# Kernel tuning notes

Measured on AMD Instinct MI355X. Metric: run time of the kernel, lower is better.

Reference implementation:

```python
import jax, jax.numpy as jnp
import numpy as np

N_NODES = 100000
N_EDGES = 800000
# (in_dim, out_channels_per_head, heads) for the 5 stacked GATConv layers
DIMS = [(32, 24, 10), (240, 24, 5), (120, 24, 2), (48, 24, 1), (24, 12, 1)]
NEG_SLOPE = 0.2  # PyG GATConv default leaky_relu slope


def setup_inputs() -> dict:
    key = jax.random.key(0)
    ks = jax.random.split(key, 4 + 4 * len(DIMS))
    x = jax.random.normal(ks[0], (N_NODES, 32), jnp.float32)
    # edge_index with no self loops (dst = src + nonzero offset mod N),
    # since PyG GATConv removes then re-adds self loops.
    src = jax.random.randint(ks[1], (N_EDGES,), 0, N_NODES)
    off = jax.random.randint(ks[2], (N_EDGES,), 1, N_NODES)
    dst = (src + off) % N_NODES
    edge_index = jnp.stack([src, dst]).astype(jnp.int32)
    edge_attr = jax.random.normal(ks[3], (N_EDGES, 4), jnp.float32)
    inp = {"x": x, "edge_index": edge_index, "edge_attr": edge_attr}
    for i, (din, c, h) in enumerate(DIMS):
        kw, kb, ka, kd = ks[4 + 4 * i: 8 + 4 * i]
        s = 1.0 / np.sqrt(din)
        inp[f"W{i}"] = jax.random.normal(kw, (din, h * c), jnp.float32) * s
        inp[f"b{i}"] = jax.random.normal(kb, (h * c,), jnp.float32) * 0.01
        inp[f"as{i}"] = jax.random.normal(ka, (h, c), jnp.float32) * (1.0 / np.sqrt(c))
        inp[f"ad{i}"] = jax.random.normal(kd, (h, c), jnp.float32) * (1.0 / np.sqrt(c))
    return inp


def gat_layer(x, src, dst, W, b, a_src, a_dst):
    # Faithful PyG GATConv (concat=True, bias=True, edge_dim=None)
    n = x.shape[0]
    h_heads, c = a_src.shape
    h = (x @ W).reshape(n, h_heads, c)                      # [N,H,C]
    alpha_s = jnp.einsum('nhc,hc->nh', h, a_src)            # [N,H]
    alpha_d = jnp.einsum('nhc,hc->nh', h, a_dst)            # [N,H]
    e = jax.nn.leaky_relu(alpha_s[src] + alpha_d[dst], NEG_SLOPE)  # [E,H]
    # segment softmax over incoming edges of each destination node
    m = jax.ops.segment_max(e, dst, num_segments=n)         # [N,H]
    ex = jnp.exp(e - m[dst])
    z = jax.ops.segment_sum(ex, dst, num_segments=n)        # [N,H]
    attn = ex / z[dst]                                      # [E,H]
    out = jax.ops.segment_sum(h[src] * attn[:, :, None], dst, num_segments=n)
    return out.reshape(n, h_heads * c) + b


def reference(x, edge_index, edge_attr,
              W0, b0, as0, ad0, W1, b1, as1, ad1, W2, b2, as2, ad2,
              W3, b3, as3, ad3, W4, b4, as4, ad4):
    # edge_attr is ignored: GATConv(edge_dim=None) does not use it.
    n = x.shape[0]
    loop = jnp.arange(n, dtype=edge_index.dtype)
    src = jnp.concatenate([edge_index[0], loop])  # add self loops (PyG default)
    dst = jnp.concatenate([edge_index[1], loop])
    params = [(W0, b0, as0, ad0), (W1, b1, as1, ad1), (W2, b2, as2, ad2),
              (W3, b3, as3, ad3), (W4, b4, as4, ad4)]
    for W, b, a_s, a_d in params:
        x = jax.nn.relu(gat_layer(x, src, dst, W, b, a_s, a_d))
    return x
```

## Files before the change

kernel.cpp:

```cpp
#include <hip/hip_runtime.h>
#include <math.h>

#define NN 100000
#define EE 800000
#define ET (EE + NN)
#define BS 256
#define BKTS 391
#define FB_EPB 4096
#define LDSCAP 4096

typedef _Float16 f16;
typedef __attribute__((ext_vector_type(2))) _Float16 h2v;
typedef __attribute__((ext_vector_type(4))) _Float16 half4;
typedef __attribute__((ext_vector_type(8))) _Float16 half8;
typedef __attribute__((ext_vector_type(4))) float f32x4;
template<int V> struct HV;
template<> struct HV<4>{ typedef half4 type; };
template<> struct HV<8>{ typedef half8 type; };

static inline int cdiv(long a, int b){ return (int)((a + b - 1) / b); }

__global__ __launch_bounds__(256) void k_bhist(const int* __restrict__ ei,
                                               int* __restrict__ bucketCount){
    __shared__ int hist[BKTS];
    for (int t = threadIdx.x; t < BKTS; t += 256) hist[t] = 0;
    __syncthreads();
    const int e0 = blockIdx.x * FB_EPB + threadIdx.x;
    #pragma unroll
    for (int i = 0; i < 16; i++){
        int e = e0 + i * 256;
        if (e < ET){
            int d = (e < EE) ? ei[EE + e] : (e - EE);
            atomicAdd(&hist[d >> 8], 1);
        }
    }
    __syncthreads();
    for (int t = threadIdx.x; t < BKTS; t += 256){
        int c = hist[t];
        if (c) atomicAdd(&bucketCount[t], c);
    }
}

__global__ void k_bscan(const int* __restrict__ bucketCount, int* __restrict__ bucketBase,
                        int* __restrict__ bucketCursor, int* __restrict__ rowptr){
    __shared__ int sh[512];
    int t = threadIdx.x;
    int c = (t < BKTS) ? bucketCount[t] : 0;
    sh[t] = c;
    __syncthreads();
    for (int o = 1; o < 512; o <<= 1){
        int v = (t >= o) ? sh[t - o] : 0;
        __syncthreads();
        sh[t] += v;
        __syncthreads();
    }
    if (t < BKTS){
        int excl = sh[t] - c;
        bucketBase[t] = excl;
        bucketCursor[t] = excl;
    }
    if (t == 0){
        bucketBase[BKTS] = ET;
        rowptr[NN] = ET;
    }
}

__global__ __launch_bounds__(256) void k_bfill(const int* __restrict__ ei,
        int* __restrict__ bucketCursor, unsigned* __restrict__ bpack){
    __shared__ int hist[BKTS];
    __shared__ int base[BKTS];
    for (int t = threadIdx.x; t < BKTS; t += 256) hist[t] = 0;
    __syncthreads();
    const int e0 = blockIdx.x * FB_EPB + threadIdx.x;
    unsigned pk[16], rb[16];
    #pragma unroll
    for (int i = 0; i < 16; i++){
        int e = e0 + i * 256;
        rb[i] = 0xFFFFFFFFu;
        if (e < ET){
            int s, d;
            if (e < EE){ s = ei[e]; d = ei[EE + e]; } else { s = e - EE; d = s; }
            int b = d >> 8;
            int r = atomicAdd(&hist[b], 1);
            pk[i] = ((unsigned)(d & 255) << 17) | (unsigned)s;
            rb[i] = ((unsigned)r << 9) | (unsigned)b;
        }
    }
    __syncthreads();
    for (int t = threadIdx.x; t < BKTS; t += 256){
        int c = hist[t];
        base[t] = c ? atomicAdd(&bucketCursor[t], c) : 0;
    }
    __syncthreads();
    #pragma unroll
    for (int i = 0; i < 16; i++){
        if (rb[i] != 0xFFFFFFFFu){
            int b = rb[i] & 511;
            int r = rb[i] >> 9;
            bpack[base[b] + r] = pk[i];
        }
    }
}

__global__ __launch_bounds__(256) void k_bsort(const unsigned* __restrict__ bpack,
        const int* __restrict__ bucketBase, int* __restrict__ rowptr,
        int* __restrict__ ssrc){
    __shared__ int cnt[256];
    __shared__ int off[256];
    __shared__ unsigned stage[LDSCAP];
    int b = blockIdx.x;
    int n0 = bucketBase[b], n1 = bucketBase[b + 1];
    int nE = n1 - n0;
    int t = threadIdx.x;
    cnt[t] = 0;
    __syncthreads();
    for (int i = t; i < nE; i += 256){
        unsigned v = bpack[n0 + i];
        atomicAdd(&cnt[v >> 17], 1);
    }
    __syncthreads();
    int cv = cnt[t];
    off[t] = cv;
    __syncthreads();
    for (int o = 1; o < 256; o <<= 1){
        int v = (t >= o) ? off[t - o] : 0;
        __syncthreads();
        off[t] += v;
        __syncthreads();
    }
    int excl = off[t] - cv;
    __syncthreads();
    off[t] = excl;
    cnt[t] = 0;
    __syncthreads();
    for (int i = t; i < nE; i += 256){
        unsigned v = bpack[n0 + i];
        int dl = v >> 17;
        int r = atomicAdd(&cnt[dl], 1);
        stage[off[dl] + r] = v;
    }
    int d = b * 256 + t;
    if (d < NN) rowptr[d] = n0 + excl;
    __syncthreads();
    for (int i = t; i < nE; i += 256){
        unsigned v = stage[i];
        ssrc[n0 + i] = (int)(v & 0x1FFFFu);
    }
}

template<int K, int M, int KP, int MP, int HH, int CC>
__device__ __forceinline__ void prep_one(int idx, const float* __restrict__ W,
        const float* __restrict__ b, const float* __restrict__ as_,
        const float* __restrict__ ad_, f16* __restrict__ Wpk,
        float* __restrict__ bp, float* __restrict__ Was, float* __restrict__ Wad){
    constexpr int NT = MP / 16;
    if (idx < KP * MP){
        int j    = idx & 7;
        int lane = (idx >> 3) & 63;
        int rest = idx >> 9;
        int nt   = rest % NT;
        int ks   = rest / NT;
        int k = ks * 32 + ((lane >> 4) & 3) * 8 + j;
        int n = nt * 16 + (lane & 15);
        Wpk[idx] = (k < K && n < M) ? (f16)W[k * M + n] : (f16)0.f;
    }
    if (idx < MP) bp[idx] = (idx < M) ? b[idx] : 0.f;
    if (idx < K * HH){
        int k = idx / HH, hd = idx - k * HH;
        float s = 0.f, d = 0.f;
        #pragma unroll
        for (int c = 0; c < CC; c++){
            float w = W[k * M + hd * CC + c];
            s = fmaf(w, as_[hd * CC + c], s);
            d = fmaf(w, ad_[hd * CC + c], d);
        }
        Was[idx] = s;
        Wad[idx] = d;
    }
}

__device__ __forceinline__ void prep_w0(int idx, const float* __restrict__ W0,
                                        f16* __restrict__ Wpk0){
    int j    = idx & 7;
    int lane = (idx >> 3) & 63;
    int nt   = (idx >> 9) & 1;
    int hd   = idx >> 10;
    int k    = ((lane >> 4) & 3) * 8 + j;
    int cih  = nt * 16 + (lane & 15);
    Wpk0[idx] = (cih < 24) ? (f16)W0[k * 240 + hd * 24 + cih] : (f16)0.f;
}

struct PrepAll {
    const float *W[5], *b[5], *as[5], *ad[5];
    f16*   Wpk[5];
    f16*   Wpk0;
    float* bp[5];
    float* Was[5];
    float* Wad[5];
    int*   bucketCount;
};

__global__ void k_prep_all(PrepAll a){
    int idx = blockIdx.x * 256 + threadIdx.x;
    if (idx < 7680)
        prep_one< 32, 240,  32, 240, 10, 24>(idx,         a.W[0], a.b[0], a.as[0], a.ad[0], a.Wpk[0], a.bp[0], a.Was[0], a.Wad[0]);
    else if (idx < 40448)
        prep_one<240, 120, 256, 128,  5, 24>(idx - 7680,  a.W[1], a.b[1], a.as[1], a.ad[1], a.Wpk[1], a.bp[1], a.Was[1], a.Wad[1]);
    else if (idx < 48640)
        prep_one<120,  48, 128,  64,  2, 24>(idx - 40448, a.W[2], a.b[2], a.as[2], a.ad[2], a.Wpk[2], a.bp[2], a.Was[2], a.Wad[2]);
    else if (idx < 50688)
        prep_one< 48,  24,  64,  32,  1, 24>(idx - 48640, a.W[3], a.b[3], a.as[3], a.ad[3], a.Wpk[3], a.bp[3], a.Was[3], a.Wad[3]);
    else if (idx < 51200)
        prep_one< 24,  12,  32,  16,  1, 12>(idx - 50688, a.W[4], a.b[4], a.as[4], a.ad[4], a.Wpk[4], a.bp[4], a.Was[4], a.Wad[4]);
    else if (idx < 61440)
        prep_w0(idx - 51200, a.W[0], a.Wpk0);
    else if (idx < 61440 + BKTS)
        a.bucketCount[idx - 61440] = 0;
}

__global__ void k_cvt_alpha0(const float* __restrict__ X, f16* __restrict__ Xh,
                             const float* __restrict__ Was, const float* __restrict__ Wad,
                             float* __restrict__ als, float* __restrict__ ald){
    int n = blockIdx.x * BS + threadIdx.x;
    if (n >= NN) return;
    float xr[32];
    #pragma unroll
    for (int i = 0; i < 8; i++){
        float4 v = *(const float4*)(X + (long)n * 32 + i * 4);
        xr[i * 4 + 0] = v.x; xr[i * 4 + 1] = v.y;
        xr[i * 4 + 2] = v.z; xr[i * 4 + 3] = v.w;
    }
    #pragma unroll
    for (int i = 0; i < 4; i++){
        half8 h;
        #pragma unroll
        for (int c = 0; c < 8; c++) h[c] = (f16)xr[i * 8 + c];
        *(half8*)(Xh + (long)n * 32 + i * 8) = h;
    }
    float s[10] = {}, d[10] = {};
    for (int k = 0; k < 32; k++){
        float x = xr[k];
        #pragma unroll
        for (int hd = 0; hd < 10; hd++){
            s[hd] = fmaf(x, Was[k * 10 + hd], s[hd]);
            d[hd] = fmaf(x, Wad[k * 10 + hd], d[hd]);
        }
    }
    #pragma unroll
    for (int hd = 0; hd < 10; hd++){
        als[(long)n * 12 + hd] = s[hd];
        ald[(long)n * 12 + hd] = d[hd];
    }
}

template<int MPH, int HH, int CC, int SL>
__global__ void k_alpha_h(const f16* __restrict__ H2, const float* __restrict__ as_,
                          const float* __restrict__ ad_, float* __restrict__ als,
                          float* __restrict__ ald){
    int n = blockIdx.x * BS + threadIdx.x;
    if (n >= NN) return;
    const f16* h = H2 + (long)n * MPH;
    #pragma unroll
    for (int hd = 0; hd < HH; hd++){
        float s = 0.f, d = 0.f;
        #pragma unroll
        for (int c0 = 0; c0 < CC; c0 += 4){
            half4 hv = *(const half4*)(h + hd * CC + c0);
            #pragma unroll
            for (int j = 0; j < 4; j++){
                float hvf = (float)hv[j];
                s = fmaf(hvf, as_[hd * CC + c0 + j], s);
                d = fmaf(hvf, ad_[hd * CC + c0 + j], d);
            }
        }
        als[(long)n * SL + hd] = s;
        ald[(long)n * SL + hd] = d;
    }
}

__device__ __forceinline__ void smx_upd(float& ma, float& L, float& z, float e, float adv){
    float mn = fmaxf(ma, e);
    float Ln = mn + adv; Ln = (Ln >= 0.f) ? Ln : 0.2f * Ln;
    float ev = e + adv;  ev = (ev >= 0.f) ? ev : 0.2f * ev;
    z = z * __expf(L - Ln) + __expf(ev - Ln);
    ma = mn; L = Ln;
}

template<int HH, int SL, int ATTS, int TPN>
__global__ __launch_bounds__(256) void k_mzatt_split(const float* __restrict__ als,
        const float* __restrict__ ald, const int* __restrict__ rowptr,
        const int* __restrict__ ssrc, f16* __restrict__ att){
    constexpr int HPT = HH / TPN;
    long idx = (long)blockIdx.x * 256 + threadIdx.x;
    if (idx >= (long)NN * TPN) return;
    int n = (int)(idx / TPN);
    int g = (int)(idx - (long)n * TPN);
    const int c0 = g * HPT;
    float adv[HPT], ma[HPT], L[HPT], z[HPT];
    #pragma unroll
    for (int h = 0; h < HPT; h++){
        adv[h] = ald[(long)n * SL + c0 + h];
        ma[h] = -1e30f; L[h] = -1e30f; z[h] = 0.f;
    }
    const int beg = rowptr[n], end = rowptr[n + 1];
    int p = beg;
    for (; p + 4 <= end; p += 4){
        int s0 = ssrc[p], s1 = ssrc[p+1], s2 = ssrc[p+2], s3 = ssrc[p+3];
        float e0[HPT], e1[HPT], e2[HPT], e3[HPT];
        if constexpr (HPT == 2){
            float2 v0 = *(const float2*)(als + (long)s0 * SL + c0);
            float2 v1 = *(const float2*)(als + (long)s1 * SL + c0);
            float2 v2 = *(const float2*)(als + (long)s2 * SL + c0);
            float2 v3 = *(const float2*)(als + (long)s3 * SL + c0);
            e0[0]=v0.x; e0[1]=v0.y; e1[0]=v1.x; e1[1]=v1.y;
            e2[0]=v2.x; e2[1]=v2.y; e3[0]=v3.x; e3[1]=v3.y;
        } else {
            e0[0] = als[(long)s0 * SL + c0];
            e1[0] = als[(long)s1 * SL + c0];
            e2[0] = als[(long)s2 * SL + c0];
            e3[0] = als[(long)s3 * SL + c0];
        }
        #pragma unroll
        for (int h = 0; h < HPT; h++){
            smx_upd(ma[h], L[h], z[h], e0[h], adv[h]);
            smx_upd(ma[h], L[h], z[h], e1[h], adv[h]);
            smx_upd(ma[h], L[h], z[h], e2[h], adv[h]);
            smx_upd(ma[h], L[h], z[h], e3[h], adv[h]);
        }
    }
    for (; p < end; ++p){
        int s = ssrc[p];
        float e[HPT];
        if constexpr (HPT == 2){
            float2 v = *(const float2*)(als + (long)s * SL + c0);
            e[0] = v.x; e[1] = v.y;
        } else {
            e[0] = als[(long)s * SL + c0];
        }
        #pragma unroll
        for (int h = 0; h < HPT; h++) smx_upd(ma[h], L[h], z[h], e[h], adv[h]);
    }
    float zi[HPT];
    int pos[HPT];
    #pragma unroll
    for (int h = 0; h < HPT; h++){
        zi[h] = 1.f / z[h];
        int hh = c0 + h;
        pos[h] = (ATTS == 16) ? (hh + ((hh >= 5) ? 3 : 0)) : hh;
    }
    auto emit = [&](int pp, const float* e){
        #pragma unroll
        for (int h = 0; h < HPT; h++){
            float ev = e[h] + adv[h]; ev = (ev >= 0.f) ? ev : 0.2f * ev;
            att[(long)pp * ATTS + pos[h]] = (f16)(__expf(ev - L[h]) * zi[h]);
        }
    };
    p = beg;
    for (; p + 4 <= end; p += 4){
        int s0 = ssrc[p], s1 = ssrc[p+1], s2 = ssrc[p+2], s3 = ssrc[p+3];
        float e0[HPT], e1[HPT], e2[HPT], e3[HPT];
        if constexpr (HPT == 2){
            float2 v0 = *(const float2*)(als + (long)s0 * SL + c0);
            float2 v1 = *(const float2*)(als + (long)s1 * SL + c0);
            float2 v2 = *(const float2*)(als + (long)s2 * SL + c0);
            float2 v3 = *(const float2*)(als + (long)s3 * SL + c0);
            e0[0]=v0.x; e0[1]=v0.y; e1[0]=v1.x; e1[1]=v1.y;
            e2[0]=v2.x; e2[1]=v2.y; e3[0]=v3.x; e3[1]=v3.y;
        } else {
            e0[0] = als[(long)s0 * SL + c0];
            e1[0] = als[(long)s1 * SL + c0];
            e2[0] = als[(long)s2 * SL + c0];
            e3[0] = als[(long)s3 * SL + c0];
        }
        emit(p, e0); emit(p+1, e1); emit(p+2, e2); emit(p+3, e3);
    }
    for (; p < end; ++p){
        int s = ssrc[p];
        float e[HPT];
        if constexpr (HPT == 2){
            float2 v = *(const float2*)(als + (long)s * SL + c0);
            e[0] = v.x; e[1] = v.y;
        } else {
            e[0] = als[(long)s * SL + c0];
        }
        emit(p, e);
    }
}

__global__ __launch_bounds__(256) void k_aggX0_gemm(const f16* __restrict__ Xh,
        const f16* __restrict__ att, const int* __restrict__ rowptr,
        const int* __restrict__ ssrc, const f16* __restrict__ Wpk0,
        const float* __restrict__ bp0, f16* __restrict__ X1){
    constexpr int SA = 328;
    constexpr int SO = 264;
    __shared__ f16 smem[32 * SA];
    const int t = threadIdx.x;
    const long n0 = (long)blockIdx.x * 32;

    {
        const int nloc = t >> 3;
        const int hg   = (t >> 2) & 1;
        const int ch   = t & 3;
        const int n    = (int)n0 + nloc;
        float acc[5][8] = {};
        int beg = rowptr[n], end = rowptr[n + 1];
        int p = beg;
        for (; p + 4 <= end; p += 4){
            int s0 = ssrc[p], s1 = ssrc[p+1], s2 = ssrc[p+2], s3 = ssrc[p+3];
            half8 x0 = *(const half8*)(Xh + (long)s0 * 32 + ch * 8);
            half8 x1 = *(const half8*)(Xh + (long)s1 * 32 + ch * 8);
            half8 x2 = *(const half8*)(Xh + (long)s2 * 32 + ch * 8);
            half8 x3 = *(const half8*)(Xh + (long)s3 * 32 + ch * 8);
            half8 a0 = *(const half8*)(att + (long)p * 16 + hg * 8);
            half8 a1 = *(const half8*)(att + (long)(p+1) * 16 + hg * 8);
            half8 a2 = *(const half8*)(att + (long)(p+2) * 16 + hg * 8);
            half8 a3 = *(const half8*)(att + (long)(p+3) * 16 + hg * 8);
            #pragma unroll
            for (int h = 0; h < 5; h++){
                float w0 = (float)a0[h], w1 = (float)a1[h];
                float w2 = (float)a2[h], w3 = (float)a3[h];
                #pragma unroll
                for (int c = 0; c < 8; c++){
                    acc[h][c] = fmaf(w0, (float)x0[c], acc[h][c]);
                    acc[h][c] = fmaf(w1, (float)x1[c], acc[h][c]);
                    acc[h][c] = fmaf(w2, (float)x2[c], acc[h][c]);
                    acc[h][c] = fmaf(w3, (float)x3[c], acc[h][c]);
                }
            }
        }
        for (; p < end; ++p){
            int s = ssrc[p];
            half8 xv = *(const half8*)(Xh + (long)s * 32 + ch * 8);
            half8 av = *(const half8*)(att + (long)p * 16 + hg * 8);
            #pragma unroll
            for (int h = 0; h < 5; h++){
                float w = (float)av[h];
                #pragma unroll
                for (int c = 0; c < 8; c++)
                    acc[h][c] = fmaf(w, (float)xv[c], acc[h][c]);
            }
        }
        #pragma unroll
        for (int h = 0; h < 5; h++){
            half8 o;
            #pragma unroll
            for (int c = 0; c < 8; c++) o[c] = (f16)acc[h][c];
            *(half8*)(smem + nloc * SA + (hg * 5 + h) * 32 + ch * 8) = o;
        }
    }
    __syncthreads();

    const int wave = t >> 6;
    const int lane = t & 63;
    const int quad = lane >> 4;
    const int l16  = lane & 15;
    const int mt   = wave & 1;
    half8 afr[5];
    #pragma unroll
    for (int i = 0; i < 5; i++){
        const int hd = (wave + 4 * i) >> 1;
        afr[i] = *(const half8*)(smem + (mt * 16 + l16) * SA + hd * 32 + quad * 8);
    }
    __syncthreads();
    #pragma unroll
    for (int i = 0; i < 5; i++){
        const int hd = (wave + 4 * i) >> 1;
        #pragma unroll
        for (int nt = 0; nt < 2; nt++){
            half8 bfr = *(const half8*)(Wpk0 + ((hd * 2 + nt) * 64 + lane) * 8);
            f32x4 acc2 = (f32x4){0.f, 0.f, 0.f, 0.f};
            acc2 = __builtin_amdgcn_mfma_f32_16x16x32_f16(afr[i], bfr, acc2, 0, 0, 0);
            int cih = nt * 16 + l16;
            if (cih < 24){
                float bv = bp0[hd * 24 + cih];
                #pragma unroll
                for (int reg = 0; reg < 4; reg++){
                    int rl = mt * 16 + quad * 4 + reg;
                    float v = acc2[reg] + bv;
                    smem[rl * SO + hd * 24 + cih] = (f16)((v > 0.f) ? v : 0.f);
                }
            }
        }
    }
    __syncthreads();

    const half8 hz = {};
    #pragma unroll
    for (int c = t; c < 1024; c += 256){
        int row = c >> 5, c8 = c & 31;
        half8 v = (c8 >= 30) ? hz : *(const half8*)(smem + row * SO + c8 * 8);
        *(half8*)(X1 + (n0 + row) * 256 + c8 * 8) = v;
    }
}

template<int KP, int MPH>
__global__ __launch_bounds__(256) void k_gemm_mfma(const f16* __restrict__ Xh,
        const f16* __restrict__ Wpk, f16* __restrict__ H2){
    constexpr int NT = MPH / 16;
    constexpr int KS = KP / 32;
    const int wave = threadIdx.x >> 6;
    const int lane = threadIdx.x & 63;
    const int quad = lane >> 4;
    const int l16  = lane & 15;
    const long row0 = (long)blockIdx.x * 128 + wave * 32;

    f32x4 acc[2][NT];
    #pragma unroll
    for (int mt = 0; mt < 2; mt++)
        #pragma unroll
        for (int nt = 0; nt < NT; nt++)
            acc[mt][nt] = (f32x4){0.f, 0.f, 0.f, 0.f};

    const long r0 = row0 + l16;
    const long r1 = row0 + 16 + l16;
    const half8 hz = {};
    half8 a0 = (r0 < NN) ? *(const half8*)(Xh + r0 * KP + quad * 8) : hz;
    half8 a1 = (r1 < NN) ? *(const half8*)(Xh + r1 * KP + quad * 8) : hz;
    half8 bc[NT];
    #pragma unroll
    for (int nt = 0; nt < NT; nt++)
        bc[nt] = *(const half8*)(Wpk + ((long)nt * 64 + lane) * 8);

    for (int ks = 0; ks < KS; ks++){
        half8 n0 = hz, n1 = hz, bn[NT];
        if (ks + 1 < KS){
            const int kk = (ks + 1) * 32 + quad * 8;
            n0 = (r0 < NN) ? *(const half8*)(Xh + r0 * KP + kk) : hz;
            n1 = (r1 < NN) ? *(const half8*)(Xh + r1 * KP + kk) : hz;
            const f16* bp_ = Wpk + ((long)(ks + 1) * NT * 64 + lane) * 8;
            #pragma unroll
            for (int nt = 0; nt < NT; nt++)
                bn[nt] = *(const half8*)(bp_ + (long)nt * 512);
        } else {
            #pragma unroll
            for (int nt = 0; nt < NT; nt++) bn[nt] = hz;
        }
        #pragma unroll
        for (int nt = 0; nt < NT; nt++){
            acc[0][nt] = __builtin_amdgcn_mfma_f32_16x16x32_f16(a0, bc[nt], acc[0][nt], 0, 0, 0);
            acc[1][nt] = __builtin_amdgcn_mfma_f32_16x16x32_f16(a1, bc[nt], acc[1][nt], 0, 0, 0);
        }
        a0 = n0; a1 = n1;
        #pragma unroll
        for (int nt = 0; nt < NT; nt++) bc[nt] = bn[nt];
    }
    #pragma unroll
    for (int mt = 0; mt < 2; mt++){
        #pragma unroll
        for (int reg = 0; reg < 4; reg++){
            long r = row0 + mt * 16 + quad * 4 + reg;
            if (r < NN){
                #pragma unroll
                for (int nt = 0; nt < NT; nt++)
                    H2[r * MPH + nt * 16 + l16] = (f16)acc[mt][nt][reg];
            }
        }
    }
}

template<int HH, int CC, int ATTS, int MPH, int MPO, int VEC, bool O16>
__global__ __launch_bounds__(256) void k_agg_h(const f16* __restrict__ H2,
        const f16* __restrict__ att,
        const int* __restrict__ rowptr, const int* __restrict__ ssrc,
        const float* __restrict__ bp, f16* __restrict__ out16,
        float* __restrict__ out32, int MREAL){
    constexpr int TPN = MPO / VEC;
    typedef typename HV<VEC>::type hvec;
    int idx = blockIdx.x * 256 + threadIdx.x;
    if (idx >= NN * TPN) return;
    int n = idx / TPN;
    int q = idx - n * TPN;
    int j0 = q * VEC;
    if constexpr (O16 && (MPO > MPH)){
        if (j0 >= MPH){
            hvec zv = {};
            *(hvec*)(out16 + (long)n * MPO + j0) = zv;
            return;
        }
    }
    int hd = j0 / CC; if (hd > HH - 1) hd = HH - 1;

    int beg = rowptr[n], end = rowptr[n + 1];
    float acc[VEC] = {};
    int p = beg;
    for (; p + 2 <= end; p += 2){
        int s0 = ssrc[p], s1 = ssrc[p + 1];
        float w0 = (float)att[(long)p * ATTS + hd];
        float w1 = (float)att[(long)(p + 1) * ATTS + hd];
        hvec h0 = *(const hvec*)(H2 + (long)s0 * MPH + j0);
        hvec h1 = *(const hvec*)(H2 + (long)s1 * MPH + j0);
        #pragma unroll
        for (int c = 0; c < VEC; c++){
            acc[c] = fmaf(w0, (float)h0[c], acc[c]);
            acc[c] = fmaf(w1, (float)h1[c], acc[c]);
        }
    }
    if (p < end){
        int s = ssrc[p];
        float w = (float)att[(long)p * ATTS + hd];
        hvec hv = *(const hvec*)(H2 + (long)s * MPH + j0);
        #pragma unroll
        for (int c = 0; c < VEC; c++)
            acc[c] = fmaf(w, (float)hv[c], acc[c]);
    }
    if constexpr (O16){
        hvec o;
        #pragma unroll
        for (int c = 0; c < VEC; c++){
            float v = acc[c] + bp[j0 + c];
            o[c] = (f16)((v > 0.f) ? v : 0.f);
        }
        *(hvec*)(out16 + (long)n * MPO + j0) = o;
    } else {
        if (j0 < MREAL){
            #pragma unroll
            for (int c = 0; c < VEC; c++){
                float v = acc[c] + bp[j0 + c];
                out32[(long)n * MREAL + j0 + c] = (v > 0.f) ? v : 0.f;
            }
        }
    }
}

template<int K, int M, int KP, int MPH, int MPO, int HH, int CC, int ATTS, int VEC,
         bool O16, int SL, int TPN>
static void run_layer(const f16* Xin, f16* H2, f16* att,
                      const f16* Wpk, const float* bp,
                      const float* asv, const float* adv,
                      float* als, float* ald,
                      const int* rowptr, const int* ssrc,
                      f16* Xnext, float* out32, hipStream_t stream){
    constexpr int OTPN = MPO / VEC;
    k_gemm_mfma<KP, MPH><<<cdiv(NN, 128), 256, 0, stream>>>(Xin, Wpk, H2);
    k_alpha_h<MPH, HH, CC, SL><<<cdiv(NN, BS), BS, 0, stream>>>(H2, asv, adv, als, ald);
    k_mzatt_split<HH, SL, ATTS, TPN><<<cdiv((long)NN * TPN, 256), 256, 0, stream>>>(
        als, ald, rowptr, ssrc, att);
    k_agg_h<HH, CC, ATTS, MPH, MPO, VEC, O16><<<cdiv((long)NN * OTPN, 256), 256, 0, stream>>>(
        H2, att, rowptr, ssrc, bp, Xnext, out32, M);
}

extern "C" void kernel_launch(void* const* d_in, const int* in_sizes, int n_in,
                              void* d_out, int out_size, void* d_ws, size_t ws_size,
                              hipStream_t stream){
    const float* x0 = (const float*)d_in[0];
    const int*   ei = (const int*)d_in[1];
    PrepAll pa;
    for (int i = 0; i < 5; i++){
        pa.W[i]  = (const float*)d_in[3 + 4 * i];
        pa.b[i]  = (const float*)d_in[4 + 4 * i];
        pa.as[i] = (const float*)d_in[5 + 4 * i];
        pa.ad[i] = (const float*)d_in[6 + 4 * i];
    }

    char* p = (char*)d_ws;
    auto alloc = [&](size_t bytes) -> char* {
        char* r = p;
        p += (bytes + 255) & ~(size_t)255;
        return r;
    };
    f16*   Xh     = (f16*)alloc((size_t)NN * 256 * 2);
    f16*   H2     = (f16*)alloc((size_t)NN * 320 * 2);
    f16*   att    = (f16*)alloc((size_t)ET * 16 * 2);
    float* als    = (float*)alloc((size_t)NN * 12 * 4);
    float* ald    = (float*)alloc((size_t)NN * 12 * 4);
    const int wpkSz[5] = {7680, 32768, 8192, 2048, 512};
    const int mpSz[5]  = {240, 128, 64, 32, 16};
    const int khSz[5]  = {320, 1200, 240, 48, 24};
    for (int i = 0; i < 5; i++){
        pa.Wpk[i] = (f16*)alloc((size_t)wpkSz[i] * 2);
        pa.bp[i]  = (float*)alloc((size_t)mpSz[i] * 4);
        pa.Was[i] = (float*)alloc((size_t)khSz[i] * 4);
        pa.Wad[i] = (float*)alloc((size_t)khSz[i] * 4);
    }
    pa.Wpk0 = (f16*)alloc((size_t)10240 * 2);
    int*      bucketCount  = (int*)alloc((size_t)BKTS * 4);
    int*      bucketBase   = (int*)alloc((size_t)(BKTS + 1) * 4);
    int*      bucketCursor = (int*)alloc((size_t)BKTS * 4);
    unsigned* bpack        = (unsigned*)alloc((size_t)ET * 4);
    int*      rowptr       = (int*)alloc((size_t)(NN + 1) * 4);
    int*      ssrc         = (int*)alloc((size_t)ET * 4);
    pa.bucketCount = bucketCount;

    k_prep_all<<<242, 256, 0, stream>>>(pa);
    k_bhist<<<cdiv(ET, FB_EPB), 256, 0, stream>>>(ei, bucketCount);
    k_bscan<<<1, 512, 0, stream>>>(bucketCount, bucketBase, bucketCursor, rowptr);
    k_bfill<<<cdiv(ET, FB_EPB), 256, 0, stream>>>(ei, bucketCursor, bpack);
    k_bsort<<<BKTS, 256, 0, stream>>>(bpack, bucketBase, rowptr, ssrc);

    k_cvt_alpha0<<<cdiv(NN, BS), BS, 0, stream>>>(x0, Xh, pa.Was[0], pa.Wad[0], als, ald);
    k_mzatt_split<10, 12, 16, 5><<<cdiv((long)NN * 5, 256), 256, 0, stream>>>(
        als, ald, rowptr, ssrc, att);
    k_aggX0_gemm<<<NN / 32, 256, 0, stream>>>(Xh, att, rowptr, ssrc,
        pa.Wpk0, pa.bp[0], H2 );

    run_layer<240, 120, 256, 128, 128,  5, 24, 8, 8, true,  8, 5>(H2, Xh, att, pa.Wpk[1],
        pa.bp[1], pa.as[1], pa.ad[1], als, ald, rowptr, ssrc, H2, nullptr, stream);
    run_layer<120,  48, 128,  64,  64,  2, 24, 2, 8, true,  2, 2>(H2, Xh, att, pa.Wpk[2],
        pa.bp[2], pa.as[2], pa.ad[2], als, ald, rowptr, ssrc, H2, nullptr, stream);
    run_layer< 48,  24,  64,  32,  32,  1, 24, 1, 8, true,  1, 1>(H2, Xh, att, pa.Wpk[3],
        pa.bp[3], pa.as[3], pa.ad[3], als, ald, rowptr, ssrc, H2, nullptr, stream);
    run_layer< 24,  12,  32,  16,  16,  1, 12, 1, 4, false, 1, 1>(H2, Xh, att, pa.Wpk[4],
        pa.bp[4], pa.as[4], pa.ad[4], als, ald, rowptr, ssrc, nullptr, (float*)d_out, stream);
}
```

Before: 452.8 us.

## Process destination nodes in degree-sorted order to balance per-node gather loops

Adds a counting sort of nodes by in-degree (histogram, scan, fill) that builds a permutation, with nodes ordered by descending degree. The softmax and aggregation kernels then index nodes through this permutation so threads within a wavefront get similar loop lengths, which is meant to reduce divergence and tail imbalance in the per-node CSR loops. It adds three small kernels and an extra indirection, and it trades coalesced, consecutive-node access to rowptr, ald and the output rows for scattered access.

```diff
diff --git a/kernel.cpp b/kernel.cpp
--- a/kernel.cpp
+++ b/kernel.cpp
@@ -8,6 +8,7 @@
 #define BKTS 391
 #define FB_EPB 4096
 #define LDSCAP 4096
+#define DBINS 64
 
 typedef _Float16 f16;
 typedef __attribute__((ext_vector_type(2))) _Float16 h2v;
@@ -146,6 +147,55 @@
         unsigned v = stage[i];
         ssrc[n0 + i] = (int)(v & 0x1FFFFu);
     }
+}
+
+__global__ __launch_bounds__(256) void k_dhist(const int* __restrict__ rowptr,
+                                               int* __restrict__ dcnt){
+    __shared__ int h[DBINS];
+    int t = threadIdx.x;
+    if (t < DBINS) h[t] = 0;
+    __syncthreads();
+    int n = blockIdx.x * 256 + t;
+    if (n < NN){
+        int d = rowptr[n + 1] - rowptr[n];
+        if (d > DBINS - 1) d = DBINS - 1;
+        atomicAdd(&h[d], 1);
+    }
+    __syncthreads();
+    if (t < DBINS && h[t]) atomicAdd(&dcnt[t], h[t]);
+}
+
+__global__ void k_dscan(const int* __restrict__ dcnt, int* __restrict__ dcur){
+    __shared__ int sh[DBINS];
+    int t = threadIdx.x;
+    sh[t] = dcnt[t];
+    __syncthreads();
+    int off = 0;
+    for (int b = t + 1; b < DBINS; ++b) off += sh[b];
+    dcur[t] = off;
+}
+
+__global__ __launch_bounds__(256) void k_dfill(const int* __restrict__ rowptr,
+        int* __restrict__ dcur, int* __restrict__ perm){
+    __shared__ int h[DBINS];
+    __shared__ int base[DBINS];
+    int t = threadIdx.x;
+    if (t < DBINS) h[t] = 0;
+    __syncthreads();
+    int n = blockIdx.x * 256 + t;
+    int d = 0, r = 0;
+    if (n < NN){
+        d = rowptr[n + 1] - rowptr[n];
+        if (d > DBINS - 1) d = DBINS - 1;
+        r = atomicAdd(&h[d], 1);
+    }
+    __syncthreads();
+    if (t < DBINS){
+        int c = h[t];
+        base[t] = c ? atomicAdd(&dcur[t], c) : 0;
+    }
+    __syncthreads();
+    if (n < NN) perm[base[d] + r] = n;
 }
 
 template<int K, int M, int KP, int MP, int HH, int CC>
@@ -198,6 +248,7 @@
     float* Was[5];
     float* Wad[5];
     int*   bucketCount;
+    int*   dcnt;
 };
 
 __global__ void k_prep_all(PrepAll a){
@@ -216,6 +267,8 @@
         prep_w0(idx - 51200, a.W[0], a.Wpk0);
     else if (idx < 61440 + BKTS)
         a.bucketCount[idx - 61440] = 0;
+    else if (idx < 61440 + BKTS + DBINS)
+        a.dcnt[idx - 61440 - BKTS] = 0;
 }
 
 __global__ void k_cvt_alpha0(const float* __restrict__ X, f16* __restrict__ Xh,
@@ -289,12 +342,13 @@
 template<int HH, int SL, int ATTS, int TPN>
 __global__ __launch_bounds__(256) void k_mzatt_split(const float* __restrict__ als,
         const float* __restrict__ ald, const int* __restrict__ rowptr,
-        const int* __restrict__ ssrc, f16* __restrict__ att){
+        const int* __restrict__ ssrc, const int* __restrict__ perm,
+        f16* __restrict__ att){
     constexpr int HPT = HH / TPN;
     long idx = (long)blockIdx.x * 256 + threadIdx.x;
     if (idx >= (long)NN * TPN) return;
-    int n = (int)(idx / TPN);
-    int g = (int)(idx - (long)n * TPN);
+    int n = perm[(int)(idx / TPN)];
+    int g = (int)(idx - (idx / TPN) * TPN);
     const int c0 = g * HPT;
     float adv[HPT], ma[HPT], L[HPT], z[HPT];
     #pragma unroll
@@ -389,19 +443,20 @@
 
 __global__ __launch_bounds__(256) void k_aggX0_gemm(const f16* __restrict__ Xh,
         const f16* __restrict__ att, const int* __restrict__ rowptr,
-        const int* __restrict__ ssrc, const f16* __restrict__ Wpk0,
-        const float* __restrict__ bp0, f16* __restrict__ X1){
+        const int* __restrict__ ssrc, const int* __restrict__ perm,
+        const f16* __restrict__ Wpk0, const float* __restrict__ bp0,
+        f16* __restrict__ X1){
     constexpr int SA = 328;
     constexpr int SO = 264;
     __shared__ f16 smem[32 * SA];
     const int t = threadIdx.x;
-    const long n0 = (long)blockIdx.x * 32;
+    const int n0 = blockIdx.x * 32;
 
     {
         const int nloc = t >> 3;
         const int hg   = (t >> 2) & 1;
         const int ch   = t & 3;
-        const int n    = (int)n0 + nloc;
+        const int n    = perm[n0 + nloc];
         float acc[5][8] = {};
         int beg = rowptr[n], end = rowptr[n + 1];
         int p = beg;
@@ -488,8 +543,9 @@
     #pragma unroll
     for (int c = t; c < 1024; c += 256){
         int row = c >> 5, c8 = c & 31;
+        long rn = perm[n0 + row];
         half8 v = (c8 >= 30) ? hz : *(const half8*)(smem + row * SO + c8 * 8);
-        *(half8*)(X1 + (n0 + row) * 256 + c8 * 8) = v;
+        *(half8*)(X1 + rn * 256 + c8 * 8) = v;
     }
 }
 
@@ -562,14 +618,15 @@
 __global__ __launch_bounds__(256) void k_agg_h(const f16* __restrict__ H2,
         const f16* __restrict__ att,
         const int* __restrict__ rowptr, const int* __restrict__ ssrc,
+        const int* __restrict__ perm,
         const float* __restrict__ bp, f16* __restrict__ out16,
         float* __restrict__ out32, int MREAL){
     constexpr int TPN = MPO / VEC;
     typedef typename HV<VEC>::type hvec;
     int idx = blockIdx.x * 256 + threadIdx.x;
     if (idx >= NN * TPN) return;
-    int n = idx / TPN;
-    int q = idx - n * TPN;
+    int n = perm[idx / TPN];
+    int q = idx - (idx / TPN) * TPN;
     int j0 = q * VEC;
     if constexpr (O16 && (MPO > MPH)){
         if (j0 >= MPH){
@@ -628,15 +685,15 @@
                       const f16* Wpk, const float* bp,
                       const float* asv, const float* adv,
                       float* als, float* ald,
-                      const int* rowptr, const int* ssrc,
+                      const int* rowptr, const int* ssrc, const int* perm,
                       f16* Xnext, float* out32, hipStream_t stream){
     constexpr int OTPN = MPO / VEC;
     k_gemm_mfma<KP, MPH><<<cdiv(NN, 128), 256, 0, stream>>>(Xin, Wpk, H2);
     k_alpha_h<MPH, HH, CC, SL><<<cdiv(NN, BS), BS, 0, stream>>>(H2, asv, adv, als, ald);
     k_mzatt_split<HH, SL, ATTS, TPN><<<cdiv((long)NN * TPN, 256), 256, 0, stream>>>(
-        als, ald, rowptr, ssrc, att);
+        als, ald, rowptr, ssrc, perm, att);
     k_agg_h<HH, CC, ATTS, MPH, MPO, VEC, O16><<<cdiv((long)NN * OTPN, 256), 256, 0, stream>>>(
-        H2, att, rowptr, ssrc, bp, Xnext, out32, M);
+        H2, att, rowptr, ssrc, perm, bp, Xnext, out32, M);
 }
 
 extern "C" void kernel_launch(void* const* d_in, const int* in_sizes, int n_in,
@@ -679,26 +736,33 @@
     unsigned* bpack        = (unsigned*)alloc((size_t)ET * 4);
     int*      rowptr       = (int*)alloc((size_t)(NN + 1) * 4);
     int*      ssrc         = (int*)alloc((size_t)ET * 4);
+    int*      dcnt         = (int*)alloc((size_t)DBINS * 4);
+    int*      dcur         = (int*)alloc((size_t)DBINS * 4);
+    int*      perm         = (int*)alloc((size_t)NN * 4);
     pa.bucketCount = bucketCount;
+    pa.dcnt = dcnt;
 
     k_prep_all<<<242, 256, 0, stream>>>(pa);
     k_bhist<<<cdiv(ET, FB_EPB), 256, 0, stream>>>(ei, bucketCount);
     k_bscan<<<1, 512, 0, stream>>>(bucketCount, bucketBase, bucketCursor, rowptr);
     k_bfill<<<cdiv(ET, FB_EPB), 256, 0, stream>>>(ei, bucketCursor, bpack);
     k_bsort<<<BKTS, 256, 0, stream>>>(bpack, bucketBase, rowptr, ssrc);
+    k_dhist<<<cdiv(NN, 256), 256, 0, stream>>>(rowptr, dcnt);
+    k_dscan<<<1, DBINS, 0, stream>>>(dcnt, dcur);
+    k_dfill<<<cdiv(NN, 256), 256, 0, stream>>>(rowptr, dcur, perm);
 
     k_cvt_alpha0<<<cdiv(NN, BS), BS, 0, stream>>>(x0, Xh, pa.Was[0], pa.Wad[0], als, ald);
     k_mzatt_split<10, 12, 16, 5><<<cdiv((long)NN * 5, 256), 256, 0, stream>>>(
-        als, ald, rowptr, ssrc, att);
-    k_aggX0_gemm<<<NN / 32, 256, 0, stream>>>(Xh, att, rowptr, ssrc,
+        als, ald, rowptr, ssrc, perm, att);
+    k_aggX0_gemm<<<NN / 32, 256, 0, stream>>>(Xh, att, rowptr, ssrc, perm,
         pa.Wpk0, pa.bp[0], H2 );
 
     run_layer<240, 120, 256, 128, 128,  5, 24, 8, 8, true,  8, 5>(H2, Xh, att, pa.Wpk[1],
-        pa.bp[1], pa.as[1], pa.ad[1], als, ald, rowptr, ssrc, H2, nullptr, stream);
+        pa.bp[1], pa.as[1], pa.ad[1], als, ald, rowptr, ssrc, perm, H2, nullptr, stream);
     run_layer<120,  48, 128,  64,  64,  2, 24, 2, 8, true,  2, 2>(H2, Xh, att, pa.Wpk[2],
-        pa.bp[2], pa.as[2], pa.ad[2], als, ald, rowptr, ssrc, H2, nullptr, stream);
+        pa.bp[2], pa.as[2], pa.ad[2], als, ald, rowptr, ssrc, perm, H2, nullptr, stream);
     run_layer< 48,  24,  64,  32,  32,  1, 24, 1, 8, true,  1, 1>(H2, Xh, att, pa.Wpk[3],
-        pa.bp[3], pa.as[3], pa.ad[3], als, ald, rowptr, ssrc, H2, nullptr, stream);
+        pa.bp[3], pa.as[3], pa.ad[3], als, ald, rowptr, ssrc, perm, H2, nullptr, stream);
     run_layer< 24,  12,  32,  16,  16,  1, 12, 1, 4, false, 1, 1>(H2, Xh, att, pa.Wpk[4],
-        pa.bp[4], pa.as[4], pa.ad[4], als, ald, rowptr, ssrc, nullptr, (float*)d_out, stream);
-}
+        pa.bp[4], pa.as[4], pa.ad[4], als, ald, rowptr, ssrc, perm, nullptr, (float*)d_out, stream);
+}
```

Measured after the change: 507.5 us. +12.1%, slower.
